# Kernel optimization log

Hardware: AMD Instinct MI355X
Metric: run time of the kernel (lower is better)

The kernel has to match this reference:

```python
import jax, jax.numpy as jnp
import numpy as np

N = 100000
E = 1600000
NEG_SLOPE = 0.2
EPS = 1e-16


def gat_layer(x, src, dst, w, W, a_src, a_dst, b):
    # x: [N, Cin] -> h: [N, Cout]
    h = x @ W
    alpha_src = h @ a_src  # [N]
    alpha_dst = h @ a_dst  # [N]
    # per-edge score: alpha_j + alpha_i, leaky relu, edge-weight adjustment
    alpha = alpha_src[src] + alpha_dst[dst]
    alpha = jax.nn.leaky_relu(alpha, NEG_SLOPE)
    alpha = alpha + (1.0 - 1.0 / w)
    # segment softmax over destination nodes
    m = jax.ops.segment_max(alpha, dst, num_segments=N)
    ea = jnp.exp(alpha - m[dst])
    denom = jax.ops.segment_sum(ea, dst, num_segments=N)
    alpha = ea / (denom[dst] + EPS)
    # scatter-add aggregation of weighted source features
    out = jax.ops.segment_sum(h[src] * alpha[:, None], dst, num_segments=N)
    return out + b


def setup_inputs() -> dict:
    key = jax.random.key(0)
    ks = jax.random.split(key, 12)
    return {
        "x": jax.random.normal(ks[0], (N, 128), dtype=jnp.float32),
        "edge_index": jax.random.randint(ks[1], (2, E), 0, N, dtype=jnp.int64)
        if jax.config.jax_enable_x64 else jax.random.randint(ks[1], (2, E), 0, N, dtype=jnp.int32),
        "edge_weight": jax.random.uniform(ks[2], (E,), dtype=jnp.float32, minval=0.5, maxval=1.5),
        "W1": jax.random.normal(ks[3], (128, 64), dtype=jnp.float32) * 0.08,
        "a_src1": jax.random.normal(ks[4], (64,), dtype=jnp.float32) * 0.1,
        "a_dst1": jax.random.normal(ks[5], (64,), dtype=jnp.float32) * 0.1,
        "b1": jax.random.normal(ks[6], (64,), dtype=jnp.float32) * 0.01,
        "W2": jax.random.normal(ks[7], (64, 7), dtype=jnp.float32) * 0.12,
        "a_src2": jax.random.normal(ks[8], (7,), dtype=jnp.float32) * 0.1,
        "a_dst2": jax.random.normal(ks[9], (7,), dtype=jnp.float32) * 0.1,
        "b2": jax.random.normal(ks[10], (7,), dtype=jnp.float32) * 0.01,
    }


def reference(x, edge_index, edge_weight, W1, a_src1, a_dst1, b1, W2, a_src2, a_dst2, b2):
    # add self loops with edge weight fill_value=1.0 (GATConv default behavior)
    loop = jnp.arange(N, dtype=edge_index.dtype)
    src = jnp.concatenate([edge_index[0], loop])
    dst = jnp.concatenate([edge_index[1], loop])
    w = jnp.concatenate([edge_weight, jnp.ones((N,), dtype=edge_weight.dtype)])
    h = gat_layer(x, src, dst, w, W1, a_src1, a_dst1, b1)
    h = jax.nn.relu(h)  # dropout is identity in eval mode
    out = gat_layer(h, src, dst, w, W2, a_src2, a_dst2, b2)
    return out
```

## Files before the change

### kernel.cpp

```cpp
#include <hip/hip_runtime.h>
#include <hip/hip_bf16.h>

typedef __hip_bfloat16 bf16;

#define DEPS 1e-16f

__device__ __forceinline__ float bfu_lo(unsigned u) { return __uint_as_float(u << 16); }
__device__ __forceinline__ float bfu_hi(unsigned u) { return __uint_as_float(u & 0xffff0000u); }

__device__ __forceinline__ float dec_wt(unsigned u) {
    return (float)(u & 32767u) * (1.f / 8192.f) - 1.1f;
}

__global__ __launch_bounds__(256) void f_gemm1(
    const float* __restrict__ x, const float* __restrict__ W1,
    const float* __restrict__ a_src, const float* __restrict__ a_dst,
    bf16* __restrict__ h1, float* __restrict__ asrc, float* __restrict__ adst,
    int N)
{
    __shared__ __align__(16) float Wl[128 * 64];
    __shared__ __align__(16) float xl[32 * 128];
    int tid = threadIdx.x;
    for (int i = tid; i < 2048; i += 256)
        ((float4*)Wl)[i] = ((const float4*)W1)[i];
    int n0 = blockIdx.x * 32;
    for (int i = tid; i < 1024; i += 256) {
        int n = n0 + (i >> 5);
        float4 v = {0.f, 0.f, 0.f, 0.f};
        if (n < N) v = ((const float4*)x)[(size_t)n * 32 + (i & 31)];
        ((float4*)xl)[i] = v;
    }
    __syncthreads();
    int w = tid >> 6, c = tid & 63;
    float sa = a_src[c], da = a_dst[c];
    float acc[8] = {0.f, 0.f, 0.f, 0.f, 0.f, 0.f, 0.f, 0.f};
    for (int k4 = 0; k4 < 32; ++k4) {
        float w0 = Wl[(4 * k4 + 0) * 64 + c];
        float w1 = Wl[(4 * k4 + 1) * 64 + c];
        float w2 = Wl[(4 * k4 + 2) * 64 + c];
        float w3 = Wl[(4 * k4 + 3) * 64 + c];
        #pragma unroll
        for (int i = 0; i < 8; ++i) {
            float4 xv = ((const float4*)(xl + (w * 8 + i) * 128))[k4];
            acc[i] = fmaf(xv.x, w0, fmaf(xv.y, w1,
                     fmaf(xv.z, w2, fmaf(xv.w, w3, acc[i]))));
        }
    }
    #pragma unroll
    for (int i = 0; i < 8; ++i) {
        int n = n0 + w * 8 + i;
        float a = acc[i];
        float ps = a * sa, pd = a * da;
        #pragma unroll
        for (int o = 32; o; o >>= 1) {
            ps += __shfl_xor(ps, o);
            pd += __shfl_xor(pd, o);
        }
        if (n < N) {
            h1[(size_t)n * 64 + c] = __float2bfloat16(a);
            if (c == 0) { asrc[n] = ps; adst[n] = pd; }
        }
    }
}

__global__ __launch_bounds__(256) void f_hist(
    const int* __restrict__ dstv, int* __restrict__ cnt,
    int* __restrict__ rank, int E, int T)
{
    int e = blockIdx.x * 256 + threadIdx.x;
    if (e >= T) return;
    int d = (e < E) ? dstv[e] : (e - E);
    rank[e] = atomicAdd(&cnt[d], 1);
}

__global__ __launch_bounds__(256) void f_scan1(
    const int* __restrict__ cnt, int* __restrict__ off,
    int* __restrict__ bsum, int N)
{
    __shared__ int sh[256];
    int i = blockIdx.x * 256 + threadIdx.x;
    int v = (i < N) ? cnt[i] : 0;
    sh[threadIdx.x] = v;
    __syncthreads();
    for (int s = 1; s < 256; s <<= 1) {
        int t = (threadIdx.x >= s) ? sh[threadIdx.x - s] : 0;
        __syncthreads();
        sh[threadIdx.x] += t;
        __syncthreads();
    }
    if (i < N) off[i + 1] = sh[threadIdx.x];
    if (threadIdx.x == 255) bsum[blockIdx.x] = sh[255];
}

__global__ __launch_bounds__(256) void f_scan2(int* __restrict__ bsum, int nb)
{
    __shared__ int sh[256];
    __shared__ int carry;
    if (threadIdx.x == 0) carry = 0;
    __syncthreads();
    for (int base = 0; base < nb; base += 256) {
        int i = base + threadIdx.x;
        int v = (i < nb) ? bsum[i] : 0;
        sh[threadIdx.x] = v;
        __syncthreads();
        for (int s = 1; s < 256; s <<= 1) {
            int t = (threadIdx.x >= s) ? sh[threadIdx.x - s] : 0;
            __syncthreads();
            sh[threadIdx.x] += t;
            __syncthreads();
        }
        if (i < nb) bsum[i] = carry + sh[threadIdx.x] - v;
        __syncthreads();
        if (threadIdx.x == 0) carry += sh[255];
        __syncthreads();
    }
}

__global__ __launch_bounds__(256) void f_scan3(
    int* __restrict__ off, const int* __restrict__ bsum, int N)
{
    int i = blockIdx.x * 256 + threadIdx.x;
    if (i < N) off[i + 1] += bsum[blockIdx.x];
    if (i == 0) off[0] = 0;
}

__global__ __launch_bounds__(256) void f_scat(
    const int* __restrict__ srcv, const int* __restrict__ dstv,
    const float* __restrict__ ew, const int* __restrict__ off,
    const int* __restrict__ rank, unsigned* __restrict__ csru, int E, int T)
{
    int e = blockIdx.x * 256 + threadIdx.x;
    if (e >= T) return;
    int s, d; float wt;
    if (e < E) { s = srcv[e]; d = dstv[e]; wt = 1.f - 1.f / ew[e]; }
    else       { s = d = e - E; wt = 0.f; }
    int pos = off[d] + rank[e];
    unsigned q = (unsigned)((wt + 1.1f) * 8192.f + 0.5f);
    csru[pos] = ((unsigned)s << 15) | q;
}

__global__ __launch_bounds__(256) void f_agg1(
    const int* __restrict__ off, const unsigned* __restrict__ csru,
    const float* __restrict__ asrc, const float* __restrict__ adst,
    const bf16* __restrict__ h1,
    const float* __restrict__ b1, const float* __restrict__ W2,
    const float* __restrict__ a2s, const float* __restrict__ a2d,
    float* __restrict__ h2p, float* __restrict__ ad2, int N)
{
    __shared__ __align__(16) float WxT[12][64];
    __shared__ __align__(16) float b1l[64];
    __shared__ float2 eb[4][64];
    int tid = threadIdx.x;
    if (tid < 64) {
        float us = 0.f, ud = 0.f;
        #pragma unroll
        for (int c = 0; c < 7; ++c) {
            float wv = W2[tid * 7 + c];
            WxT[c][tid] = wv;
            us = fmaf(wv, a2s[c], us);
            ud = fmaf(wv, a2d[c], ud);
        }
        WxT[7][tid] = us;
        WxT[8][tid] = ud;
        WxT[9][tid] = 0.f; WxT[10][tid] = 0.f; WxT[11][tid] = 0.f;
        b1l[tid] = b1[tid];
    }
    __syncthreads();
    int d = blockIdx.x * 4 + (tid >> 6);
    int lane = tid & 63;
    if (d >= N) return;
    int r0 = off[d], r1 = off[d + 1];
    float adv = adst[d];
    int g = lane >> 4, l16 = lane & 15;
    float2* ebw = eb[tid >> 6];
    float acc0 = 0.f, acc1 = 0.f, acc2 = 0.f, acc3 = 0.f, sm = 0.f;
    for (int base = r0; base < r1; base += 64) {
        int p = base + lane;
        float ea = 0.f; unsigned s = 0;
        if (p < r1) {
            unsigned u = csru[p];
            s = u >> 15;
            float a = asrc[s] + adv;
            a = (a > 0.f) ? a : 0.2f * a;
            ea = __expf(a + dec_wt(u));
            sm += ea;
        }
        ebw[lane] = make_float2(ea, __uint_as_float(s));
        int nc = min(64, r1 - base);
        for (int j = 0; j < nc; j += 4) {
            float2 eq = ebw[j + g];
            float e = eq.x;
            unsigned sj = __float_as_uint(eq.y);
            uint2 hv = *(const uint2*)&h1[(size_t)sj * 64 + (l16 << 2)];
            acc0 = fmaf(e, bfu_lo(hv.x), acc0);
            acc1 = fmaf(e, bfu_hi(hv.x), acc1);
            acc2 = fmaf(e, bfu_lo(hv.y), acc2);
            acc3 = fmaf(e, bfu_hi(hv.y), acc3);
        }
    }
    #pragma unroll
    for (int o = 32; o; o >>= 1) sm += __shfl_xor(sm, o);
    acc0 += __shfl_xor(acc0, 16); acc0 += __shfl_xor(acc0, 32);
    acc1 += __shfl_xor(acc1, 16); acc1 += __shfl_xor(acc1, 32);
    acc2 += __shfl_xor(acc2, 16); acc2 += __shfl_xor(acc2, 32);
    acc3 += __shfl_xor(acc3, 16); acc3 += __shfl_xor(acc3, 32);
    float inv = 1.f / (sm + DEPS);
    int c0 = 4 * l16;
    float4 bb = *(const float4*)&b1l[c0];
    float v0 = fmaxf(fmaf(acc0, inv, bb.x), 0.f);
    float v1 = fmaxf(fmaf(acc1, inv, bb.y), 0.f);
    float v2 = fmaxf(fmaf(acc2, inv, bb.z), 0.f);
    float v3 = fmaxf(fmaf(acc3, inv, bb.w), 0.f);
    int colb = g * 3;
    float4 w0 = *(const float4*)&WxT[colb][c0];
    float4 w1 = *(const float4*)&WxT[colb + 1][c0];
    float4 w2 = *(const float4*)&WxT[colb + 2][c0];
    float r0v = fmaf(v0, w0.x, fmaf(v1, w0.y, fmaf(v2, w0.z, v3 * w0.w)));
    float r1v = fmaf(v0, w1.x, fmaf(v1, w1.y, fmaf(v2, w1.z, v3 * w1.w)));
    float r2v = fmaf(v0, w2.x, fmaf(v1, w2.y, fmaf(v2, w2.z, v3 * w2.w)));
    #pragma unroll
    for (int o = 8; o; o >>= 1) {
        r0v += __shfl_xor(r0v, o);
        r1v += __shfl_xor(r1v, o);
        r2v += __shfl_xor(r2v, o);
    }
    if (l16 == 0) {
        float* row = &h2p[(size_t)d * 8];
        if (g == 0)      { row[0] = r0v; row[1] = r1v; row[2] = r2v; }
        else if (g == 1) { row[3] = r0v; row[4] = r1v; row[5] = r2v; }
        else if (g == 2) { row[6] = r0v; row[7] = r1v; ad2[d] = r2v; }
    }
}

__global__ __launch_bounds__(256) void f_agg2(
    const int* __restrict__ off, const unsigned* __restrict__ csru,
    const float* __restrict__ h2p, const float* __restrict__ ad2,
    const float* __restrict__ b2, float* __restrict__ out, int N)
{
    __shared__ float b2l[7];
    if (threadIdx.x < 7) b2l[threadIdx.x] = b2[threadIdx.x];
    __syncthreads();
    int lane = threadIdx.x & 63;
    int wv = threadIdx.x >> 6;
    int grp = lane >> 3, l8 = lane & 7;
    int d = blockIdx.x * 32 + wv * 8 + grp;
    bool valid = d < N;
    int r0 = 0, r1 = 0; float adv = 0.f;
    if (valid) { r0 = off[d]; r1 = off[d + 1]; adv = ad2[d]; }
    float sm = 0.f;
    float a0 = 0.f, a1 = 0.f, a2 = 0.f, a3 = 0.f, a4 = 0.f, a5 = 0.f, a6 = 0.f;
    for (int p = r0 + l8; p < r1; p += 8) {
        unsigned u = csru[p];
        int s = (int)(u >> 15);
        const float* hr = &h2p[(size_t)s * 8];
        float4 A = *(const float4*)hr;
        float4 B = *(const float4*)(hr + 4);
        float a = B.w + adv;
        a = (a > 0.f) ? a : 0.2f * a;
        float ea = __expf(a + dec_wt(u));
        sm += ea;
        a0 = fmaf(ea, A.x, a0); a1 = fmaf(ea, A.y, a1);
        a2 = fmaf(ea, A.z, a2); a3 = fmaf(ea, A.w, a3);
        a4 = fmaf(ea, B.x, a4); a5 = fmaf(ea, B.y, a5);
        a6 = fmaf(ea, B.z, a6);
    }
    #pragma unroll
    for (int o = 4; o; o >>= 1) {
        sm += __shfl_xor(sm, o);
        a0 += __shfl_xor(a0, o); a1 += __shfl_xor(a1, o);
        a2 += __shfl_xor(a2, o); a3 += __shfl_xor(a3, o);
        a4 += __shfl_xor(a4, o); a5 += __shfl_xor(a5, o);
        a6 += __shfl_xor(a6, o);
    }
    if (valid && l8 < 7) {
        float inv = 1.f / (sm + DEPS);
        float val = (l8 < 4) ? ((l8 < 2) ? (l8 ? a1 : a0) : ((l8 == 2) ? a2 : a3))
                             : ((l8 < 6) ? ((l8 == 4) ? a4 : a5) : a6);
        out[(size_t)d * 7 + l8] = fmaf(val, inv, b2l[l8]);
    }
}


extern "C" void kernel_launch(void* const* d_in, const int* in_sizes, int n_in,
                              void* d_out, int out_size, void* d_ws, size_t ws_size,
                              hipStream_t stream) {
    const float* x   = (const float*)d_in[0];
    const int*   ei  = (const int*)d_in[1];
    const float* ew  = (const float*)d_in[2];
    const float* W1  = (const float*)d_in[3];
    const float* as1 = (const float*)d_in[4];
    const float* ad1 = (const float*)d_in[5];
    const float* b1  = (const float*)d_in[6];
    const float* W2  = (const float*)d_in[7];
    const float* a2s = (const float*)d_in[8];
    const float* a2d = (const float*)d_in[9];
    const float* b2  = (const float*)d_in[10];

    int N = in_sizes[0] / 128;
    int E = in_sizes[1] / 2;
    int T = E + N;
    const int* srcv = ei;
    const int* dstv = ei + E;
    float* out = (float*)d_out;

    int gT  = (T + 255) / 256;
    int gN  = (N + 255) / 256;
    int nb1 = gN;

    size_t A = 0;
    auto take = [&](size_t b) { size_t o = A; A = (A + b + 255) & ~(size_t)255; return o; };
    size_t o_h1   = take((size_t)N * 64 * 2);
    size_t o_csr  = take((size_t)T * 4);
    size_t o_rank = take((size_t)T * 4);
    size_t o_off  = take((size_t)(N + 1) * 4);
    size_t o_cnt  = take((size_t)N * 4);
    size_t o_asrc = take((size_t)N * 4);
    size_t o_adst = take((size_t)N * 4);
    size_t o_ad2  = take((size_t)N * 4);
    size_t o_h2p  = take((size_t)N * 8 * 4);
    size_t o_bsum = take((size_t)nb1 * 4);

    char* base = (char*)d_ws;
    bf16*     h1     = (bf16*)(base + o_h1);
    unsigned* csru   = (unsigned*)(base + o_csr);
    int*      rank   = (int*)(base + o_rank);
    int*      off    = (int*)(base + o_off);
    int*      cnt    = (int*)(base + o_cnt);
    float*    asrc   = (float*)(base + o_asrc);
    float*    adst   = (float*)(base + o_adst);
    float*    ad2    = (float*)(base + o_ad2);
    float*    h2p    = (float*)(base + o_h2p);
    int*      bsum   = (int*)(base + o_bsum);

    hipMemsetAsync(cnt, 0, (size_t)N * 4, stream);
    f_hist<<<gT, 256, 0, stream>>>(dstv, cnt, rank, E, T);
    f_scan1<<<nb1, 256, 0, stream>>>(cnt, off, bsum, N);
    f_scan2<<<1, 256, 0, stream>>>(bsum, nb1);
    f_scan3<<<nb1, 256, 0, stream>>>(off, bsum, N);
    f_scat<<<gT, 256, 0, stream>>>(srcv, dstv, ew, off, rank, csru, E, T);
    f_gemm1<<<(N + 31) / 32, 256, 0, stream>>>(x, W1, as1, ad1, h1, asrc, adst, N);
    f_agg1<<<(N + 3) / 4, 256, 0, stream>>>(off, csru, asrc, adst, h1,
                                            b1, W2, a2s, a2d, h2p, ad2, N);
    f_agg2<<<(N + 31) / 32, 256, 0, stream>>>(off, csru, h2p, ad2, b2, out, N);
}
```

Baseline: 339.0 us.

## Replace CSR build with fixed-capacity per-node buckets plus overflow list

Drops the histogram, three-pass prefix scan and rank-based scatter used to build a CSR by destination. Each edge now claims a slot with a single atomicAdd into a fixed 32-entry bucket per node, and edges beyond that capacity go to a global overflow list. Both aggregation kernels read the bucket directly and, only for nodes with more than 32 edges, scan the whole overflow list for matching entries. This removes several launches and a full pass over the edges, at the cost of a larger, sparser adjacency buffer. It also risks silently dropping edges if the overflow exceeds OVF_MAX, and makes high-degree nodes slow because the overflow scan is linear.

```diff
diff --git a/kernel.cpp b/kernel.cpp
--- a/kernel.cpp
+++ b/kernel.cpp
@@ -4,6 +4,8 @@
 typedef __hip_bfloat16 bf16;
 
 #define DEPS 1e-16f
+#define CAP 32
+#define OVF_MAX 131072
 
 __device__ __forceinline__ float bfu_lo(unsigned u) { return __uint_as_float(u << 16); }
 __device__ __forceinline__ float bfu_hi(unsigned u) { return __uint_as_float(u & 0xffff0000u); }
@@ -63,84 +65,31 @@
     }
 }
 
-__global__ __launch_bounds__(256) void f_hist(
-    const int* __restrict__ dstv, int* __restrict__ cnt,
-    int* __restrict__ rank, int E, int T)
-{
-    int e = blockIdx.x * 256 + threadIdx.x;
-    if (e >= T) return;
-    int d = (e < E) ? dstv[e] : (e - E);
-    rank[e] = atomicAdd(&cnt[d], 1);
-}
-
-__global__ __launch_bounds__(256) void f_scan1(
-    const int* __restrict__ cnt, int* __restrict__ off,
-    int* __restrict__ bsum, int N)
-{
-    __shared__ int sh[256];
-    int i = blockIdx.x * 256 + threadIdx.x;
-    int v = (i < N) ? cnt[i] : 0;
-    sh[threadIdx.x] = v;
-    __syncthreads();
-    for (int s = 1; s < 256; s <<= 1) {
-        int t = (threadIdx.x >= s) ? sh[threadIdx.x - s] : 0;
-        __syncthreads();
-        sh[threadIdx.x] += t;
-        __syncthreads();
-    }
-    if (i < N) off[i + 1] = sh[threadIdx.x];
-    if (threadIdx.x == 255) bsum[blockIdx.x] = sh[255];
-}
-
-__global__ __launch_bounds__(256) void f_scan2(int* __restrict__ bsum, int nb)
-{
-    __shared__ int sh[256];
-    __shared__ int carry;
-    if (threadIdx.x == 0) carry = 0;
-    __syncthreads();
-    for (int base = 0; base < nb; base += 256) {
-        int i = base + threadIdx.x;
-        int v = (i < nb) ? bsum[i] : 0;
-        sh[threadIdx.x] = v;
-        __syncthreads();
-        for (int s = 1; s < 256; s <<= 1) {
-            int t = (threadIdx.x >= s) ? sh[threadIdx.x - s] : 0;
-            __syncthreads();
-            sh[threadIdx.x] += t;
-            __syncthreads();
-        }
-        if (i < nb) bsum[i] = carry + sh[threadIdx.x] - v;
-        __syncthreads();
-        if (threadIdx.x == 0) carry += sh[255];
-        __syncthreads();
-    }
-}
-
-__global__ __launch_bounds__(256) void f_scan3(
-    int* __restrict__ off, const int* __restrict__ bsum, int N)
-{
-    int i = blockIdx.x * 256 + threadIdx.x;
-    if (i < N) off[i + 1] += bsum[blockIdx.x];
-    if (i == 0) off[0] = 0;
-}
-
-__global__ __launch_bounds__(256) void f_scat(
+__global__ __launch_bounds__(256) void f_bucket(
     const int* __restrict__ srcv, const int* __restrict__ dstv,
-    const float* __restrict__ ew, const int* __restrict__ off,
-    const int* __restrict__ rank, unsigned* __restrict__ csru, int E, int T)
+    const float* __restrict__ ew, int* __restrict__ cnt,
+    unsigned* __restrict__ bkt, uint2* __restrict__ ovf,
+    int* __restrict__ ovfn, int E, int T)
 {
     int e = blockIdx.x * 256 + threadIdx.x;
     if (e >= T) return;
     int s, d; float wt;
     if (e < E) { s = srcv[e]; d = dstv[e]; wt = 1.f - 1.f / ew[e]; }
     else       { s = d = e - E; wt = 0.f; }
-    int pos = off[d] + rank[e];
     unsigned q = (unsigned)((wt + 1.1f) * 8192.f + 0.5f);
-    csru[pos] = ((unsigned)s << 15) | q;
+    unsigned entry = ((unsigned)s << 15) | q;
+    int pos = atomicAdd(&cnt[d], 1);
+    if (pos < CAP) {
+        bkt[(size_t)d * CAP + pos] = entry;
+    } else {
+        int o = atomicAdd(ovfn, 1);
+        if (o < OVF_MAX) { uint2 v; v.x = (unsigned)d; v.y = entry; ovf[o] = v; }
+    }
 }
 
 __global__ __launch_bounds__(256) void f_agg1(
-    const int* __restrict__ off, const unsigned* __restrict__ csru,
+    const int* __restrict__ cnt, const unsigned* __restrict__ bkt,
+    const uint2* __restrict__ ovf, const int* __restrict__ ovfn,
     const float* __restrict__ asrc, const float* __restrict__ adst,
     const bf16* __restrict__ h1,
     const float* __restrict__ b1, const float* __restrict__ W2,
@@ -169,16 +118,17 @@
     int d = blockIdx.x * 4 + (tid >> 6);
     int lane = tid & 63;
     if (d >= N) return;
-    int r0 = off[d], r1 = off[d + 1];
+    int lenf = cnt[d];
+    int nc = min(lenf, CAP);
+    size_t r0 = (size_t)d * CAP;
     float adv = adst[d];
     int g = lane >> 4, l16 = lane & 15;
     float2* ebw = eb[tid >> 6];
     float acc0 = 0.f, acc1 = 0.f, acc2 = 0.f, acc3 = 0.f, sm = 0.f;
-    for (int base = r0; base < r1; base += 64) {
-        int p = base + lane;
+    {
         float ea = 0.f; unsigned s = 0;
-        if (p < r1) {
-            unsigned u = csru[p];
+        if (lane < nc) {
+            unsigned u = bkt[r0 + lane];
             s = u >> 15;
             float a = asrc[s] + adv;
             a = (a > 0.f) ? a : 0.2f * a;
@@ -186,7 +136,6 @@
             sm += ea;
         }
         ebw[lane] = make_float2(ea, __uint_as_float(s));
-        int nc = min(64, r1 - base);
         for (int j = 0; j < nc; j += 4) {
             float2 eq = ebw[j + g];
             float e = eq.x;
@@ -196,6 +145,25 @@
             acc1 = fmaf(e, bfu_hi(hv.x), acc1);
             acc2 = fmaf(e, bfu_lo(hv.y), acc2);
             acc3 = fmaf(e, bfu_hi(hv.y), acc3);
+        }
+    }
+    if (lenf > CAP) {
+        int no = min(*ovfn, OVF_MAX);
+        for (int i = g; i < no; i += 4) {
+            uint2 ov = ovf[i];
+            if ((int)ov.x == d) {
+                unsigned u = ov.y;
+                unsigned s = u >> 15;
+                float a = asrc[s] + adv;
+                a = (a > 0.f) ? a : 0.2f * a;
+                float ea = __expf(a + dec_wt(u));
+                if (l16 == 0) sm += ea;
+                uint2 hv = *(const uint2*)&h1[(size_t)s * 64 + (l16 << 2)];
+                acc0 = fmaf(ea, bfu_lo(hv.x), acc0);
+                acc1 = fmaf(ea, bfu_hi(hv.x), acc1);
+                acc2 = fmaf(ea, bfu_lo(hv.y), acc2);
+                acc3 = fmaf(ea, bfu_hi(hv.y), acc3);
+            }
         }
     }
     #pragma unroll
@@ -233,7 +201,8 @@
 }
 
 __global__ __launch_bounds__(256) void f_agg2(
-    const int* __restrict__ off, const unsigned* __restrict__ csru,
+    const int* __restrict__ cnt, const unsigned* __restrict__ bkt,
+    const uint2* __restrict__ ovf, const int* __restrict__ ovfn,
     const float* __restrict__ h2p, const float* __restrict__ ad2,
     const float* __restrict__ b2, float* __restrict__ out, int N)
 {
@@ -245,12 +214,14 @@
     int grp = lane >> 3, l8 = lane & 7;
     int d = blockIdx.x * 32 + wv * 8 + grp;
     bool valid = d < N;
-    int r0 = 0, r1 = 0; float adv = 0.f;
-    if (valid) { r0 = off[d]; r1 = off[d + 1]; adv = ad2[d]; }
+    int lenf = 0; float adv = 0.f;
+    if (valid) { lenf = cnt[d]; adv = ad2[d]; }
+    int nc = min(lenf, CAP);
+    size_t r0 = (size_t)d * CAP;
     float sm = 0.f;
     float a0 = 0.f, a1 = 0.f, a2 = 0.f, a3 = 0.f, a4 = 0.f, a5 = 0.f, a6 = 0.f;
-    for (int p = r0 + l8; p < r1; p += 8) {
-        unsigned u = csru[p];
+    for (int p = l8; p < nc; p += 8) {
+        unsigned u = bkt[r0 + p];
         int s = (int)(u >> 15);
         const float* hr = &h2p[(size_t)s * 8];
         float4 A = *(const float4*)hr;
@@ -263,6 +234,27 @@
         a2 = fmaf(ea, A.z, a2); a3 = fmaf(ea, A.w, a3);
         a4 = fmaf(ea, B.x, a4); a5 = fmaf(ea, B.y, a5);
         a6 = fmaf(ea, B.z, a6);
+    }
+    if (lenf > CAP) {
+        int no = min(*ovfn, OVF_MAX);
+        for (int i = l8; i < no; i += 8) {
+            uint2 ov = ovf[i];
+            if ((int)ov.x == d) {
+                unsigned u = ov.y;
+                int s = (int)(u >> 15);
+                const float* hr = &h2p[(size_t)s * 8];
+                float4 A = *(const float4*)hr;
+                float4 B = *(const float4*)(hr + 4);
+                float a = B.w + adv;
+                a = (a > 0.f) ? a : 0.2f * a;
+                float ea = __expf(a + dec_wt(u));
+                sm += ea;
+                a0 = fmaf(ea, A.x, a0); a1 = fmaf(ea, A.y, a1);
+                a2 = fmaf(ea, A.z, a2); a3 = fmaf(ea, A.w, a3);
+                a4 = fmaf(ea, B.x, a4); a5 = fmaf(ea, B.y, a5);
+                a6 = fmaf(ea, B.z, a6);
+            }
+        }
     }
     #pragma unroll
     for (int o = 4; o; o >>= 1) {
@@ -303,43 +295,35 @@
     const int* dstv = ei + E;
     float* out = (float*)d_out;
 
-    int gT  = (T + 255) / 256;
-    int gN  = (N + 255) / 256;
-    int nb1 = gN;
+    int gT = (T + 255) / 256;
 
     size_t A = 0;
     auto take = [&](size_t b) { size_t o = A; A = (A + b + 255) & ~(size_t)255; return o; };
     size_t o_h1   = take((size_t)N * 64 * 2);
-    size_t o_csr  = take((size_t)T * 4);
-    size_t o_rank = take((size_t)T * 4);
-    size_t o_off  = take((size_t)(N + 1) * 4);
+    size_t o_bkt  = take((size_t)N * CAP * 4);
+    size_t o_h2p  = take((size_t)N * 8 * 4);
+    size_t o_ovf  = take((size_t)OVF_MAX * 8);
     size_t o_cnt  = take((size_t)N * 4);
+    size_t o_ovfn = take(256);
     size_t o_asrc = take((size_t)N * 4);
     size_t o_adst = take((size_t)N * 4);
     size_t o_ad2  = take((size_t)N * 4);
-    size_t o_h2p  = take((size_t)N * 8 * 4);
-    size_t o_bsum = take((size_t)nb1 * 4);
 
     char* base = (char*)d_ws;
-    bf16*     h1     = (bf16*)(base + o_h1);
-    unsigned* csru   = (unsigned*)(base + o_csr);
-    int*      rank   = (int*)(base + o_rank);
-    int*      off    = (int*)(base + o_off);
-    int*      cnt    = (int*)(base + o_cnt);
-    float*    asrc   = (float*)(base + o_asrc);
-    float*    adst   = (float*)(base + o_adst);
-    float*    ad2    = (float*)(base + o_ad2);
-    float*    h2p    = (float*)(base + o_h2p);
-    int*      bsum   = (int*)(base + o_bsum);
-
-    hipMemsetAsync(cnt, 0, (size_t)N * 4, stream);
-    f_hist<<<gT, 256, 0, stream>>>(dstv, cnt, rank, E, T);
-    f_scan1<<<nb1, 256, 0, stream>>>(cnt, off, bsum, N);
-    f_scan2<<<1, 256, 0, stream>>>(bsum, nb1);
-    f_scan3<<<nb1, 256, 0, stream>>>(off, bsum, N);
-    f_scat<<<gT, 256, 0, stream>>>(srcv, dstv, ew, off, rank, csru, E, T);
+    bf16*     h1   = (bf16*)(base + o_h1);
+    unsigned* bkt  = (unsigned*)(base + o_bkt);
+    float*    h2p  = (float*)(base + o_h2p);
+    uint2*    ovf  = (uint2*)(base + o_ovf);
+    int*      cnt  = (int*)(base + o_cnt);
+    int*      ovfn = (int*)(base + o_ovfn);
+    float*    asrc = (float*)(base + o_asrc);
+    float*    adst = (float*)(base + o_adst);
+    float*    ad2  = (float*)(base + o_ad2);
+
+    hipMemsetAsync(cnt, 0, (size_t)N * 4 + 256, stream);
+    f_bucket<<<gT, 256, 0, stream>>>(srcv, dstv, ew, cnt, bkt, ovf, ovfn, E, T);
     f_gemm1<<<(N + 31) / 32, 256, 0, stream>>>(x, W1, as1, ad1, h1, asrc, adst, N);
-    f_agg1<<<(N + 3) / 4, 256, 0, stream>>>(off, csru, asrc, adst, h1,
+    f_agg1<<<(N + 3) / 4, 256, 0, stream>>>(cnt, bkt, ovf, ovfn, asrc, adst, h1,
                                             b1, W2, a2s, a2d, h2p, ad2, N);
-    f_agg2<<<(N + 31) / 32, 256, 0, stream>>>(off, csru, h2p, ad2, b2, out, N);
-}
+    f_agg2<<<(N + 31) / 32, 256, 0, stream>>>(cnt, bkt, ovf, ovfn, h2p, ad2, b2, out, N);
+}
```

Result: slower. 350.9 us (+3.5%).
